# Kernel optimization log

Hardware: AMD Instinct MI355X
Metric: run time of the kernel (lower is better)

The kernel has to match this reference:

```python
import jax, jax.numpy as jnp
import numpy as np

NUM_ITER = 6  # matches init kwarg num_iter
N = 8388608


def setup_inputs() -> dict:
    key = jax.random.key(0)
    k1, k2 = jax.random.split(key, 2)
    # ray origins on plane x = -30, lateral extent inside the 50mm aperture
    yz = jax.random.uniform(k1, (N, 2), jnp.float32, -22.0, 22.0)
    P = jnp.concatenate([jnp.full((N, 1), -30.0, jnp.float32), yz], axis=1)
    # nearly-paraxial directions along +x, normalized
    dv = 0.05 * jax.random.normal(k2, (N, 2), jnp.float32)
    V = jnp.concatenate([jnp.ones((N, 1), jnp.float32), dv], axis=1)
    V = V / jnp.linalg.norm(V, axis=1, keepdims=True)
    tf_in = jnp.eye(4, dtype=jnp.float32)
    return {
        'P': P, 'V': V, 'tf_in': tf_in,
        'diameter': jnp.asarray(50.0, jnp.float32),
        'C': jnp.asarray(0.02, jnp.float32),
        'anchors': jnp.zeros((2,), jnp.float32),
        'scale': jnp.asarray(1.0, jnp.float32),
    }


def _translate_x(dx, dtype):
    return jnp.eye(4, dtype=dtype).at[0, 3].set(dx)


def reference(P, V, tf_in, diameter, C, anchors, scale):
    dtype = P.dtype

    def sag(y, z):
        # spherical sag: s(r) = C r^2 / (1 + sqrt(1 - C^2 r^2)); ds/dy = y*C/sqrt(.), ds/dz = z*C/sqrt(.)
        r2 = y * y + z * z
        sq = jnp.sqrt(jnp.clip(1.0 - C * C * r2, 1e-12))
        return C * r2 / (1.0 + sq), C / sq

    zero = jnp.zeros((), dtype)
    ext0, _ = sag(anchors[0] * diameter * 0.5, zero)
    ext1, _ = sag(anchors[1] * diameter * 0.5, zero)

    one = jnp.ones((), dtype)
    S = jnp.diag(jnp.stack([scale, scale, scale, one]))
    tf_surface = tf_in @ _translate_x(-scale * ext0, dtype) @ S
    tf_next = tf_in @ _translate_x(scale * (ext1 - ext0), dtype)

    M = tf_surface[:3, :3]
    b = tf_surface[:3, 3]
    Minv = jnp.linalg.inv(M)
    Pl = (P - b) @ Minv.T   # rays in local surface frame
    Vl = V @ Minv.T

    def F_grad(t):
        Q = Pl + t[:, None] * Vl           # [N,3] current iterate
        sv, d = sag(Q[:, 1], Q[:, 2])
        F = sv - Q[:, 0]                   # implicit residual: sag(y,z) - x
        g = jnp.stack([-jnp.ones_like(F), d * Q[:, 1], d * Q[:, 2]], axis=1)
        return Q, F, g

    def step(t, _):
        _, F, g = F_grad(t)
        denom = jnp.sum(g * Vl, axis=1)
        denom = jnp.where(jnp.abs(denom) > 1e-12, denom, 1e-12)
        return t - F / denom, None

    t0 = jnp.zeros(P.shape[0], dtype)
    t, _ = jax.lax.scan(step, t0, None, length=NUM_ITER)

    Q, F, g = F_grad(t)
    r2 = Q[:, 1] ** 2 + Q[:, 2] ** 2
    valid = (r2 <= (diameter * 0.5) ** 2) & (jnp.abs(F) < 1e-3) & (C * C * r2 < 1.0)

    nl = g / jnp.linalg.norm(g, axis=1, keepdims=True)
    n = nl @ Minv                          # normals transform by M^{-T}
    n = n / jnp.linalg.norm(n, axis=1, keepdims=True)
    return t, n, valid, tf_surface, tf_next
```

## Files before the change

kernel.cpp:

```cpp
#include <hip/hip_runtime.h>
#include <math.h>

__global__ void setup_k(const float* __restrict__ tf_in,
                        const float* __restrict__ diameter,
                        const float* __restrict__ C,
                        const float* __restrict__ anchors,
                        const float* __restrict__ scale,
                        float* __restrict__ tf_out,
                        float* __restrict__ ws) {
    float Cv = C[0], dia = diameter[0], sc = scale[0];
    float a0 = anchors[0] * dia * 0.5f;
    float a1 = anchors[1] * dia * 0.5f;
    float r20 = a0 * a0, r21 = a1 * a1;
    float sq0 = sqrtf(fmaxf(1.0f - Cv * Cv * r20, 1e-12f));
    float sq1 = sqrtf(fmaxf(1.0f - Cv * Cv * r21, 1e-12f));
    float ext0 = Cv * r20 / (1.0f + sq0);
    float ext1 = Cv * r21 / (1.0f + sq1);
    float dx0 = -sc * ext0;
    float dx1 = sc * (ext1 - ext0);

    float M[9], b[3];
    for (int r = 0; r < 4; ++r) {
        float t0 = tf_in[r*4+0], t1 = tf_in[r*4+1], t2 = tf_in[r*4+2], t3 = tf_in[r*4+3];
        tf_out[r*4+0] = t0 * sc;
        tf_out[r*4+1] = t1 * sc;
        tf_out[r*4+2] = t2 * sc;
        tf_out[r*4+3] = t0 * dx0 + t3;
        tf_out[16 + r*4+0] = t0;
        tf_out[16 + r*4+1] = t1;
        tf_out[16 + r*4+2] = t2;
        tf_out[16 + r*4+3] = t0 * dx1 + t3;
        if (r < 3) {
            M[r*3+0] = t0 * sc; M[r*3+1] = t1 * sc; M[r*3+2] = t2 * sc;
            b[r] = t0 * dx0 + t3;
        }
    }
    float c00 =  (M[4]*M[8] - M[5]*M[7]);
    float c01 = -(M[3]*M[8] - M[5]*M[6]);
    float c02 =  (M[3]*M[7] - M[4]*M[6]);
    float det = M[0]*c00 + M[1]*c01 + M[2]*c02;
    float id = 1.0f / det;
    float inv[9];
    inv[0] =  c00 * id;
    inv[1] = -(M[1]*M[8] - M[2]*M[7]) * id;
    inv[2] =  (M[1]*M[5] - M[2]*M[4]) * id;
    inv[3] =  c01 * id;
    inv[4] =  (M[0]*M[8] - M[2]*M[6]) * id;
    inv[5] = -(M[0]*M[5] - M[2]*M[3]) * id;
    inv[6] =  c02 * id;
    inv[7] = -(M[0]*M[7] - M[1]*M[6]) * id;
    inv[8] =  (M[0]*M[4] - M[1]*M[3]) * id;
    #pragma unroll
    for (int i = 0; i < 9; ++i) ws[i] = inv[i];
    ws[9]  = b[0]; ws[10] = b[1]; ws[11] = b[2];
    ws[12] = Cv;
    ws[13] = (dia * 0.5f) * (dia * 0.5f);
    ws[14] = Cv * Cv;
    ws[15] = 1.0f / Cv;
}

__device__ __forceinline__ float frcp(float x) { return __builtin_amdgcn_rcpf(x); }
__device__ __forceinline__ float frsq(float x) { return __builtin_amdgcn_rsqf(x); }

typedef float fx4 __attribute__((ext_vector_type(4)));

struct v4 { float a, b, c, d; };
__device__ __forceinline__ v4 vsub(v4 x, v4 y) { return {x.a-y.a, x.b-y.b, x.c-y.c, x.d-y.d}; }
__device__ __forceinline__ v4 vmul(v4 x, v4 y) { return {x.a*y.a, x.b*y.b, x.c*y.c, x.d*y.d}; }
__device__ __forceinline__ v4 vmuls(v4 x, float s) { return {x.a*s, x.b*s, x.c*s, x.d*s}; }
__device__ __forceinline__ v4 vfma(v4 x, v4 y, v4 z) {
    return {fmaf(x.a,y.a,z.a), fmaf(x.b,y.b,z.b), fmaf(x.c,y.c,z.c), fmaf(x.d,y.d,z.d)};
}
__device__ __forceinline__ v4 vfmas(v4 x, float s, v4 z) {
    return {fmaf(x.a,s,z.a), fmaf(x.b,s,z.b), fmaf(x.c,s,z.c), fmaf(x.d,s,z.d)};
}
__device__ __forceinline__ v4 vmaxs(v4 x, float s) {
    return {fmaxf(x.a,s), fmaxf(x.b,s), fmaxf(x.c,s), fmaxf(x.d,s)};
}
__device__ __forceinline__ v4 vrsq(v4 x) { return {frsq(x.a), frsq(x.b), frsq(x.c), frsq(x.d)}; }
__device__ __forceinline__ v4 vrcp(v4 x) { return {frcp(x.a), frcp(x.b), frcp(x.c), frcp(x.d)}; }
__device__ __forceinline__ v4 vneg(v4 x) { return {-x.a, -x.b, -x.c, -x.d}; }
__device__ __forceinline__ float clampden(float x) { return (fabsf(x) > 1e-12f) ? x : 1e-12f; }
__device__ __forceinline__ v4 vclampden(v4 x) {
    return {clampden(x.a), clampden(x.b), clampden(x.c), clampden(x.d)};
}

__global__ __launch_bounds__(256) void trace_k(
    const float4* __restrict__ P4, const float4* __restrict__ V4,
    const float* __restrict__ ws,
    float* __restrict__ t_out, fx4* __restrict__ n_out4,
    float* __restrict__ valid_out, int ntiles) {
    __shared__ float sB[3072];
    fx4* sB4 = (fx4*)sB;
    const int tid = threadIdx.x;
    const int blk = blockIdx.x;
    if (blk >= ntiles) return;

    const size_t fbase = (size_t)blk * 768;

    float4 pr0 = P4[fbase + 0*256 + tid];
    float4 pr1 = P4[fbase + 1*256 + tid];
    float4 pr2 = P4[fbase + 2*256 + tid];
    float4 vr0 = V4[fbase + 0*256 + tid];
    float4 vr1 = V4[fbase + 1*256 + tid];
    float4 vr2 = V4[fbase + 2*256 + tid];

    const float m00 = ws[0], m01 = ws[1], m02 = ws[2];
    const float m10 = ws[3], m11 = ws[4], m12 = ws[5];
    const float m20 = ws[6], m21 = ws[7], m22 = ws[8];
    const float b0 = ws[9], b1 = ws[10], b2 = ws[11];
    const float Cv = ws[12], rmax2 = ws[13], cc = ws[14], invC = ws[15];

    sB4[0*256 + tid] = (fx4){pr0.x, pr0.y, pr0.z, pr0.w};
    sB4[1*256 + tid] = (fx4){pr1.x, pr1.y, pr1.z, pr1.w};
    sB4[2*256 + tid] = (fx4){pr2.x, pr2.y, pr2.z, pr2.w};
    __syncthreads();
    float Pl0a[4], Pl1a[4], Pl2a[4];
    #pragma unroll
    for (int k = 0; k < 4; ++k) {
        const int el = k*256 + tid;
        float dpx = sB[el*3+0] - b0;
        float dpy = sB[el*3+1] - b1;
        float dpz = sB[el*3+2] - b2;
        Pl0a[k] = fmaf(dpx, m00, fmaf(dpy, m01, dpz*m02));
        Pl1a[k] = fmaf(dpx, m10, fmaf(dpy, m11, dpz*m12));
        Pl2a[k] = fmaf(dpx, m20, fmaf(dpy, m21, dpz*m22));
    }
    __syncthreads();

    sB4[0*256 + tid] = (fx4){vr0.x, vr0.y, vr0.z, vr0.w};
    sB4[1*256 + tid] = (fx4){vr1.x, vr1.y, vr1.z, vr1.w};
    sB4[2*256 + tid] = (fx4){vr2.x, vr2.y, vr2.z, vr2.w};
    __syncthreads();
    float Vl0a[4], Vl1a[4], Vl2a[4];
    #pragma unroll
    for (int k = 0; k < 4; ++k) {
        const int el = k*256 + tid;
        float wx = sB[el*3+0], wy = sB[el*3+1], wz = sB[el*3+2];
        Vl0a[k] = fmaf(wx, m00, fmaf(wy, m01, wz*m02));
        Vl1a[k] = fmaf(wx, m10, fmaf(wy, m11, wz*m12));
        Vl2a[k] = fmaf(wx, m20, fmaf(wy, m21, wz*m22));
    }
    __syncthreads();

    v4 Pl0 = {Pl0a[0], Pl0a[1], Pl0a[2], Pl0a[3]};
    v4 Pl1 = {Pl1a[0], Pl1a[1], Pl1a[2], Pl1a[3]};
    v4 Pl2 = {Pl2a[0], Pl2a[1], Pl2a[2], Pl2a[3]};
    v4 Vl0 = {Vl0a[0], Vl0a[1], Vl0a[2], Vl0a[3]};
    v4 Vl1 = {Vl1a[0], Vl1a[1], Vl1a[2], Vl1a[3]};
    v4 Vl2 = {Vl2a[0], Vl2a[1], Vl2a[2], Vl2a[3]};

    const v4 one = {1.0f, 1.0f, 1.0f, 1.0f};
    v4 t = {0.0f, 0.0f, 0.0f, 0.0f};
    #pragma unroll
    for (int it = 0; it < 6; ++it) {
        v4 q1 = vfma(t, Vl1, Pl1);
        v4 q2 = vfma(t, Vl2, Pl2);
        v4 r2 = vfma(q1, q1, vmul(q2, q2));
        v4 w  = vmaxs(vfmas(r2, -cc, one), 1e-12f);
        v4 rs = vrsq(w);
        v4 sq = vmul(w, rs);
        v4 d  = vmuls(rs, Cv);
        v4 sv = vfmas(sq, -invC, {invC, invC, invC, invC});
        v4 q0 = vfma(t, Vl0, Pl0);
        v4 F  = vsub(sv, q0);
        v4 dot = vfma(q2, Vl2, vmul(q1, Vl1));
        v4 denom = vclampden(vfma(d, dot, vneg(Vl0)));
        t = vfma(vneg(F), vrcp(denom), t);
    }
    v4 q0 = vfma(t, Vl0, Pl0);
    v4 q1 = vfma(t, Vl1, Pl1);
    v4 q2 = vfma(t, Vl2, Pl2);
    v4 r2 = vfma(q1, q1, vmul(q2, q2));
    v4 wp = vfmas(r2, -cc, one);
    v4 w  = vmaxs(wp, 1e-12f);
    v4 rs = vrsq(w);
    v4 sq = vmul(w, rs);
    v4 d  = vmuls(rs, Cv);
    v4 sv = vfmas(sq, -invC, {invC, invC, invC, invC});
    v4 F  = vsub(sv, q0);

    v4 g1 = vmul(d, q1), g2 = vmul(d, q2);
    v4 nm00 = {-m00,-m00,-m00,-m00}, nm01 = {-m01,-m01,-m01,-m01}, nm02 = {-m02,-m02,-m02,-m02};
    v4 n0 = vfmas(g1, m10, vfmas(g2, m20, nm00));
    v4 n1 = vfmas(g1, m11, vfmas(g2, m21, nm01));
    v4 n2 = vfmas(g1, m12, vfmas(g2, m22, nm02));
    v4 ninv = vrsq(vfma(n0, n0, vfma(n1, n1, vmul(n2, n2))));
    n0 = vmul(n0, ninv); n1 = vmul(n1, ninv); n2 = vmul(n2, ninv);

    float ta[4]  = {t.a, t.b, t.c, t.d};
    float n0a[4] = {n0.a, n0.b, n0.c, n0.d};
    float n1a[4] = {n1.a, n1.b, n1.c, n1.d};
    float n2a[4] = {n2.a, n2.b, n2.c, n2.d};
    float r2a[4] = {r2.a, r2.b, r2.c, r2.d};
    float Fa[4]  = {F.a, F.b, F.c, F.d};
    float wpa[4] = {wp.a, wp.b, wp.c, wp.d};

    const size_t ebase = (size_t)blk * 1024;
    #pragma unroll
    for (int k = 0; k < 4; ++k) {
        const int el = k*256 + tid;
        sB[el*3+0] = n0a[k];
        sB[el*3+1] = n1a[k];
        sB[el*3+2] = n2a[k];
        float vd = (r2a[k] <= rmax2 && fabsf(Fa[k]) < 0.001f && wpa[k] > 0.0f) ? 1.0f : 0.0f;
        __builtin_nontemporal_store(ta[k], &t_out[ebase + el]);
        __builtin_nontemporal_store(vd, &valid_out[ebase + el]);
    }
    __syncthreads();

    __builtin_nontemporal_store(sB4[0*256 + tid], &n_out4[fbase + 0*256 + tid]);
    __builtin_nontemporal_store(sB4[1*256 + tid], &n_out4[fbase + 1*256 + tid]);
    __builtin_nontemporal_store(sB4[2*256 + tid], &n_out4[fbase + 2*256 + tid]);
}

__global__ void trace_tail_k(const float* __restrict__ P, const float* __restrict__ V,
                             const float* __restrict__ ws,
                             float* __restrict__ t_out, float* __restrict__ n_out,
                             float* __restrict__ valid_out, int start, int N) {
    int i = start + blockIdx.x * blockDim.x + threadIdx.x;
    if (i >= N) return;
    const float m00 = ws[0], m01 = ws[1], m02 = ws[2];
    const float m10 = ws[3], m11 = ws[4], m12 = ws[5];
    const float m20 = ws[6], m21 = ws[7], m22 = ws[8];
    const float b0 = ws[9], b1 = ws[10], b2 = ws[11];
    const float Cv = ws[12], rmax2 = ws[13], cc = ws[14], invC = ws[15];
    float dpx = P[i*3+0] - b0, dpy = P[i*3+1] - b1, dpz = P[i*3+2] - b2;
    float Pl0 = m00*dpx + m01*dpy + m02*dpz;
    float Pl1 = m10*dpx + m11*dpy + m12*dpz;
    float Pl2 = m20*dpx + m21*dpy + m22*dpz;
    float Vl0 = m00*V[i*3+0] + m01*V[i*3+1] + m02*V[i*3+2];
    float Vl1 = m10*V[i*3+0] + m11*V[i*3+1] + m12*V[i*3+2];
    float Vl2 = m20*V[i*3+0] + m21*V[i*3+1] + m22*V[i*3+2];
    float t = 0.0f;
    for (int it = 0; it < 6; ++it) {
        float q1 = Pl1 + t*Vl1, q2 = Pl2 + t*Vl2;
        float r2 = q1*q1 + q2*q2;
        float w  = fmaxf(1.0f - cc*r2, 1e-12f);
        float rs = frsq(w);
        float sq = w * rs;
        float d  = Cv * rs;
        float sv = fmaf(sq, -invC, invC);
        float F  = sv - (Pl0 + t*Vl0);
        float denom = d*(q1*Vl1 + q2*Vl2) - Vl0;
        denom = (fabsf(denom) > 1e-12f) ? denom : 1e-12f;
        t = t - F * frcp(denom);
    }
    float q0 = Pl0 + t*Vl0, q1 = Pl1 + t*Vl1, q2 = Pl2 + t*Vl2;
    float r2 = q1*q1 + q2*q2;
    float wp = 1.0f - cc*r2;
    float w  = fmaxf(wp, 1e-12f);
    float rs = frsq(w);
    float sq = w * rs;
    float d  = Cv * rs;
    float sv = fmaf(sq, -invC, invC);
    float F  = sv - q0;
    bool valid = (r2 <= rmax2) && (fabsf(F) < 0.001f) && (wp > 0.0f);
    float g1 = d*q1, g2 = d*q2;
    float n0 = -m00 + g1*m10 + g2*m20;
    float n1 = -m01 + g1*m11 + g2*m21;
    float n2 = -m02 + g1*m12 + g2*m22;
    float ninv = frsq(n0*n0 + n1*n1 + n2*n2);
    t_out[i] = t;
    n_out[i*3+0] = n0*ninv; n_out[i*3+1] = n1*ninv; n_out[i*3+2] = n2*ninv;
    valid_out[i] = valid ? 1.0f : 0.0f;
}

extern "C" void kernel_launch(void* const* d_in, const int* in_sizes, int n_in,
                              void* d_out, int out_size, void* d_ws, size_t ws_size,
                              hipStream_t stream) {
    const float* P       = (const float*)d_in[0];
    const float* V       = (const float*)d_in[1];
    const float* tf_in   = (const float*)d_in[2];
    const float* dia     = (const float*)d_in[3];
    const float* C       = (const float*)d_in[4];
    const float* anchors = (const float*)d_in[5];
    const float* scale   = (const float*)d_in[6];
    const int N = in_sizes[0] / 3;

    float* out = (float*)d_out;
    float* ws  = (float*)d_ws;

    float* t_out     = out;
    float* n_out     = out + (size_t)N;
    float* valid_out = out + (size_t)4*N;
    float* tf_out    = out + (size_t)5*N;

    setup_k<<<1, 1, 0, stream>>>(tf_in, dia, C, anchors, scale, tf_out, ws);

    const int ntiles = N / 1024;
    if (ntiles > 0) {
        trace_k<<<ntiles, 256, 0, stream>>>((const float4*)P, (const float4*)V, ws,
                                            t_out, (fx4*)n_out, valid_out, ntiles);
    }
    const int start = ntiles * 1024;
    const int rem = N - start;
    if (rem > 0) {
        trace_tail_k<<<(rem + 255) / 256, 256, 0, stream>>>(P, V, ws, t_out, n_out,
                                                            valid_out, start, N);
    }
}
```

Baseline: 66.44 us.

## Make trace kernel persistent with grid-stride tiles and register prefetch of next tile

The trace kernel now launches at most 2048 blocks that loop over tiles in grid-stride fashion. While the current tile is being computed, the P and V loads for the next tile are issued into registers, so global loads overlap the Newton iterations and stores. The aim is to hide memory latency and cut block launch overhead for this bandwidth-bound kernel. In exchange it uses more registers per thread and so may lower occupancy, and the fixed grid size can leave the load unbalanced across CUs.

```diff
diff --git a/kernel.cpp b/kernel.cpp
--- a/kernel.cpp
+++ b/kernel.cpp
@@ -93,17 +93,10 @@
     __shared__ float sB[3072];
     fx4* sB4 = (fx4*)sB;
     const int tid = threadIdx.x;
-    const int blk = blockIdx.x;
-    if (blk >= ntiles) return;
-
-    const size_t fbase = (size_t)blk * 768;
-
-    float4 pr0 = P4[fbase + 0*256 + tid];
-    float4 pr1 = P4[fbase + 1*256 + tid];
-    float4 pr2 = P4[fbase + 2*256 + tid];
-    float4 vr0 = V4[fbase + 0*256 + tid];
-    float4 vr1 = V4[fbase + 1*256 + tid];
-    float4 vr2 = V4[fbase + 2*256 + tid];
+    const int G = gridDim.x;
+
+    int tile = blockIdx.x;
+    if (tile >= ntiles) return;
 
     const float m00 = ws[0], m01 = ws[1], m02 = ws[2];
     const float m10 = ws[3], m11 = ws[4], m12 = ws[5];
@@ -111,107 +104,134 @@
     const float b0 = ws[9], b1 = ws[10], b2 = ws[11];
     const float Cv = ws[12], rmax2 = ws[13], cc = ws[14], invC = ws[15];
 
-    sB4[0*256 + tid] = (fx4){pr0.x, pr0.y, pr0.z, pr0.w};
-    sB4[1*256 + tid] = (fx4){pr1.x, pr1.y, pr1.z, pr1.w};
-    sB4[2*256 + tid] = (fx4){pr2.x, pr2.y, pr2.z, pr2.w};
-    __syncthreads();
-    float Pl0a[4], Pl1a[4], Pl2a[4];
-    #pragma unroll
-    for (int k = 0; k < 4; ++k) {
-        const int el = k*256 + tid;
-        float dpx = sB[el*3+0] - b0;
-        float dpy = sB[el*3+1] - b1;
-        float dpz = sB[el*3+2] - b2;
-        Pl0a[k] = fmaf(dpx, m00, fmaf(dpy, m01, dpz*m02));
-        Pl1a[k] = fmaf(dpx, m10, fmaf(dpy, m11, dpz*m12));
-        Pl2a[k] = fmaf(dpx, m20, fmaf(dpy, m21, dpz*m22));
-    }
-    __syncthreads();
-
-    sB4[0*256 + tid] = (fx4){vr0.x, vr0.y, vr0.z, vr0.w};
-    sB4[1*256 + tid] = (fx4){vr1.x, vr1.y, vr1.z, vr1.w};
-    sB4[2*256 + tid] = (fx4){vr2.x, vr2.y, vr2.z, vr2.w};
-    __syncthreads();
-    float Vl0a[4], Vl1a[4], Vl2a[4];
-    #pragma unroll
-    for (int k = 0; k < 4; ++k) {
-        const int el = k*256 + tid;
-        float wx = sB[el*3+0], wy = sB[el*3+1], wz = sB[el*3+2];
-        Vl0a[k] = fmaf(wx, m00, fmaf(wy, m01, wz*m02));
-        Vl1a[k] = fmaf(wx, m10, fmaf(wy, m11, wz*m12));
-        Vl2a[k] = fmaf(wx, m20, fmaf(wy, m21, wz*m22));
-    }
-    __syncthreads();
-
-    v4 Pl0 = {Pl0a[0], Pl0a[1], Pl0a[2], Pl0a[3]};
-    v4 Pl1 = {Pl1a[0], Pl1a[1], Pl1a[2], Pl1a[3]};
-    v4 Pl2 = {Pl2a[0], Pl2a[1], Pl2a[2], Pl2a[3]};
-    v4 Vl0 = {Vl0a[0], Vl0a[1], Vl0a[2], Vl0a[3]};
-    v4 Vl1 = {Vl1a[0], Vl1a[1], Vl1a[2], Vl1a[3]};
-    v4 Vl2 = {Vl2a[0], Vl2a[1], Vl2a[2], Vl2a[3]};
-
-    const v4 one = {1.0f, 1.0f, 1.0f, 1.0f};
-    v4 t = {0.0f, 0.0f, 0.0f, 0.0f};
-    #pragma unroll
-    for (int it = 0; it < 6; ++it) {
+    size_t fb = (size_t)tile * 768;
+    float4 pr0 = P4[fb + 0*256 + tid];
+    float4 pr1 = P4[fb + 1*256 + tid];
+    float4 pr2 = P4[fb + 2*256 + tid];
+    float4 vr0 = V4[fb + 0*256 + tid];
+    float4 vr1 = V4[fb + 1*256 + tid];
+    float4 vr2 = V4[fb + 2*256 + tid];
+
+    while (true) {
+        const size_t fbase = (size_t)tile * 768;
+        const size_t ebase = (size_t)tile * 1024;
+        const int next = tile + G;
+
+        sB4[0*256 + tid] = (fx4){pr0.x, pr0.y, pr0.z, pr0.w};
+        sB4[1*256 + tid] = (fx4){pr1.x, pr1.y, pr1.z, pr1.w};
+        sB4[2*256 + tid] = (fx4){pr2.x, pr2.y, pr2.z, pr2.w};
+        __syncthreads();
+        float Pl0a[4], Pl1a[4], Pl2a[4];
+        #pragma unroll
+        for (int k = 0; k < 4; ++k) {
+            const int el = k*256 + tid;
+            float dpx = sB[el*3+0] - b0;
+            float dpy = sB[el*3+1] - b1;
+            float dpz = sB[el*3+2] - b2;
+            Pl0a[k] = fmaf(dpx, m00, fmaf(dpy, m01, dpz*m02));
+            Pl1a[k] = fmaf(dpx, m10, fmaf(dpy, m11, dpz*m12));
+            Pl2a[k] = fmaf(dpx, m20, fmaf(dpy, m21, dpz*m22));
+        }
+        __syncthreads();
+
+        sB4[0*256 + tid] = (fx4){vr0.x, vr0.y, vr0.z, vr0.w};
+        sB4[1*256 + tid] = (fx4){vr1.x, vr1.y, vr1.z, vr1.w};
+        sB4[2*256 + tid] = (fx4){vr2.x, vr2.y, vr2.z, vr2.w};
+        __syncthreads();
+        float Vl0a[4], Vl1a[4], Vl2a[4];
+        #pragma unroll
+        for (int k = 0; k < 4; ++k) {
+            const int el = k*256 + tid;
+            float wx = sB[el*3+0], wy = sB[el*3+1], wz = sB[el*3+2];
+            Vl0a[k] = fmaf(wx, m00, fmaf(wy, m01, wz*m02));
+            Vl1a[k] = fmaf(wx, m10, fmaf(wy, m11, wz*m12));
+            Vl2a[k] = fmaf(wx, m20, fmaf(wy, m21, wz*m22));
+        }
+        __syncthreads();
+
+        if (next < ntiles) {
+            const size_t fb2 = (size_t)next * 768;
+            pr0 = P4[fb2 + 0*256 + tid];
+            pr1 = P4[fb2 + 1*256 + tid];
+            pr2 = P4[fb2 + 2*256 + tid];
+            vr0 = V4[fb2 + 0*256 + tid];
+            vr1 = V4[fb2 + 1*256 + tid];
+            vr2 = V4[fb2 + 2*256 + tid];
+        }
+
+        v4 Pl0 = {Pl0a[0], Pl0a[1], Pl0a[2], Pl0a[3]};
+        v4 Pl1 = {Pl1a[0], Pl1a[1], Pl1a[2], Pl1a[3]};
+        v4 Pl2 = {Pl2a[0], Pl2a[1], Pl2a[2], Pl2a[3]};
+        v4 Vl0 = {Vl0a[0], Vl0a[1], Vl0a[2], Vl0a[3]};
+        v4 Vl1 = {Vl1a[0], Vl1a[1], Vl1a[2], Vl1a[3]};
+        v4 Vl2 = {Vl2a[0], Vl2a[1], Vl2a[2], Vl2a[3]};
+
+        const v4 one = {1.0f, 1.0f, 1.0f, 1.0f};
+        v4 t = {0.0f, 0.0f, 0.0f, 0.0f};
+        #pragma unroll
+        for (int it = 0; it < 6; ++it) {
+            v4 q1 = vfma(t, Vl1, Pl1);
+            v4 q2 = vfma(t, Vl2, Pl2);
+            v4 r2 = vfma(q1, q1, vmul(q2, q2));
+            v4 w  = vmaxs(vfmas(r2, -cc, one), 1e-12f);
+            v4 rs = vrsq(w);
+            v4 sq = vmul(w, rs);
+            v4 d  = vmuls(rs, Cv);
+            v4 sv = vfmas(sq, -invC, {invC, invC, invC, invC});
+            v4 q0 = vfma(t, Vl0, Pl0);
+            v4 F  = vsub(sv, q0);
+            v4 dot = vfma(q2, Vl2, vmul(q1, Vl1));
+            v4 denom = vclampden(vfma(d, dot, vneg(Vl0)));
+            t = vfma(vneg(F), vrcp(denom), t);
+        }
+        v4 q0 = vfma(t, Vl0, Pl0);
         v4 q1 = vfma(t, Vl1, Pl1);
         v4 q2 = vfma(t, Vl2, Pl2);
         v4 r2 = vfma(q1, q1, vmul(q2, q2));
-        v4 w  = vmaxs(vfmas(r2, -cc, one), 1e-12f);
+        v4 wp = vfmas(r2, -cc, one);
+        v4 w  = vmaxs(wp, 1e-12f);
         v4 rs = vrsq(w);
         v4 sq = vmul(w, rs);
         v4 d  = vmuls(rs, Cv);
         v4 sv = vfmas(sq, -invC, {invC, invC, invC, invC});
-        v4 q0 = vfma(t, Vl0, Pl0);
         v4 F  = vsub(sv, q0);
-        v4 dot = vfma(q2, Vl2, vmul(q1, Vl1));
-        v4 denom = vclampden(vfma(d, dot, vneg(Vl0)));
-        t = vfma(vneg(F), vrcp(denom), t);
-    }
-    v4 q0 = vfma(t, Vl0, Pl0);
-    v4 q1 = vfma(t, Vl1, Pl1);
-    v4 q2 = vfma(t, Vl2, Pl2);
-    v4 r2 = vfma(q1, q1, vmul(q2, q2));
-    v4 wp = vfmas(r2, -cc, one);
-    v4 w  = vmaxs(wp, 1e-12f);
-    v4 rs = vrsq(w);
-    v4 sq = vmul(w, rs);
-    v4 d  = vmuls(rs, Cv);
-    v4 sv = vfmas(sq, -invC, {invC, invC, invC, invC});
-    v4 F  = vsub(sv, q0);
-
-    v4 g1 = vmul(d, q1), g2 = vmul(d, q2);
-    v4 nm00 = {-m00,-m00,-m00,-m00}, nm01 = {-m01,-m01,-m01,-m01}, nm02 = {-m02,-m02,-m02,-m02};
-    v4 n0 = vfmas(g1, m10, vfmas(g2, m20, nm00));
-    v4 n1 = vfmas(g1, m11, vfmas(g2, m21, nm01));
-    v4 n2 = vfmas(g1, m12, vfmas(g2, m22, nm02));
-    v4 ninv = vrsq(vfma(n0, n0, vfma(n1, n1, vmul(n2, n2))));
-    n0 = vmul(n0, ninv); n1 = vmul(n1, ninv); n2 = vmul(n2, ninv);
-
-    float ta[4]  = {t.a, t.b, t.c, t.d};
-    float n0a[4] = {n0.a, n0.b, n0.c, n0.d};
-    float n1a[4] = {n1.a, n1.b, n1.c, n1.d};
-    float n2a[4] = {n2.a, n2.b, n2.c, n2.d};
-    float r2a[4] = {r2.a, r2.b, r2.c, r2.d};
-    float Fa[4]  = {F.a, F.b, F.c, F.d};
-    float wpa[4] = {wp.a, wp.b, wp.c, wp.d};
-
-    const size_t ebase = (size_t)blk * 1024;
-    #pragma unroll
-    for (int k = 0; k < 4; ++k) {
-        const int el = k*256 + tid;
-        sB[el*3+0] = n0a[k];
-        sB[el*3+1] = n1a[k];
-        sB[el*3+2] = n2a[k];
-        float vd = (r2a[k] <= rmax2 && fabsf(Fa[k]) < 0.001f && wpa[k] > 0.0f) ? 1.0f : 0.0f;
-        __builtin_nontemporal_store(ta[k], &t_out[ebase + el]);
-        __builtin_nontemporal_store(vd, &valid_out[ebase + el]);
-    }
-    __syncthreads();
-
-    __builtin_nontemporal_store(sB4[0*256 + tid], &n_out4[fbase + 0*256 + tid]);
-    __builtin_nontemporal_store(sB4[1*256 + tid], &n_out4[fbase + 1*256 + tid]);
-    __builtin_nontemporal_store(sB4[2*256 + tid], &n_out4[fbase + 2*256 + tid]);
+
+        v4 g1 = vmul(d, q1), g2 = vmul(d, q2);
+        v4 nm00 = {-m00,-m00,-m00,-m00}, nm01 = {-m01,-m01,-m01,-m01}, nm02 = {-m02,-m02,-m02,-m02};
+        v4 n0 = vfmas(g1, m10, vfmas(g2, m20, nm00));
+        v4 n1 = vfmas(g1, m11, vfmas(g2, m21, nm01));
+        v4 n2 = vfmas(g1, m12, vfmas(g2, m22, nm02));
+        v4 ninv = vrsq(vfma(n0, n0, vfma(n1, n1, vmul(n2, n2))));
+        n0 = vmul(n0, ninv); n1 = vmul(n1, ninv); n2 = vmul(n2, ninv);
+
+        float ta[4]  = {t.a, t.b, t.c, t.d};
+        float n0a[4] = {n0.a, n0.b, n0.c, n0.d};
+        float n1a[4] = {n1.a, n1.b, n1.c, n1.d};
+        float n2a[4] = {n2.a, n2.b, n2.c, n2.d};
+        float r2a[4] = {r2.a, r2.b, r2.c, r2.d};
+        float Fa[4]  = {F.a, F.b, F.c, F.d};
+        float wpa[4] = {wp.a, wp.b, wp.c, wp.d};
+
+        #pragma unroll
+        for (int k = 0; k < 4; ++k) {
+            const int el = k*256 + tid;
+            sB[el*3+0] = n0a[k];
+            sB[el*3+1] = n1a[k];
+            sB[el*3+2] = n2a[k];
+            float vd = (r2a[k] <= rmax2 && fabsf(Fa[k]) < 0.001f && wpa[k] > 0.0f) ? 1.0f : 0.0f;
+            __builtin_nontemporal_store(ta[k], &t_out[ebase + el]);
+            __builtin_nontemporal_store(vd, &valid_out[ebase + el]);
+        }
+        __syncthreads();
+
+        __builtin_nontemporal_store(sB4[0*256 + tid], &n_out4[fbase + 0*256 + tid]);
+        __builtin_nontemporal_store(sB4[1*256 + tid], &n_out4[fbase + 1*256 + tid]);
+        __builtin_nontemporal_store(sB4[2*256 + tid], &n_out4[fbase + 2*256 + tid]);
+
+        if (next >= ntiles) break;
+        tile = next;
+        __syncthreads();
+    }
 }
 
 __global__ void trace_tail_k(const float* __restrict__ P, const float* __restrict__ V,
@@ -290,8 +310,9 @@
 
     const int ntiles = N / 1024;
     if (ntiles > 0) {
-        trace_k<<<ntiles, 256, 0, stream>>>((const float4*)P, (const float4*)V, ws,
-                                            t_out, (fx4*)n_out, valid_out, ntiles);
+        const int grid = (ntiles < 2048) ? ntiles : 2048;
+        trace_k<<<grid, 256, 0, stream>>>((const float4*)P, (const float4*)V, ws,
+                                          t_out, (fx4*)n_out, valid_out, ntiles);
     }
     const int start = ntiles * 1024;
     const int rem = N - start;
```

Result: slower. 68.27 us (+2.8%).
